# Optimization experiments

Measured on AMD Instinct MI355X. Metric: run time of the kernel, lower is better.

## Reference

```python
import jax, jax.numpy as jnp
import numpy as np

B, S, N_WIRES, EMBED_DIM, NUM_HEADS = 4, 2048, 8, 512, 8
D_K = EMBED_DIM // NUM_HEADS


def setup_inputs() -> dict:
    key = jax.random.key(0)
    k_x, k_th, k_q, k_k, k_v, k_c = jax.random.split(key, 6)
    x = jax.random.normal(k_x, (B, S, N_WIRES), dtype=jnp.float32)
    # trainable RX rotation angles, one per wire
    theta = jax.random.normal(k_th, (N_WIRES,), dtype=jnp.float32) * 0.1
    # nn.Linear(n_wires, embed_dim, bias=False) weights have shape (embed_dim, n_wires)
    sc_in = 1.0 / np.sqrt(N_WIRES)
    Wq = jax.random.normal(k_q, (EMBED_DIM, N_WIRES), dtype=jnp.float32) * sc_in
    Wk = jax.random.normal(k_k, (EMBED_DIM, N_WIRES), dtype=jnp.float32) * sc_in
    Wv = jax.random.normal(k_v, (EMBED_DIM, N_WIRES), dtype=jnp.float32) * sc_in
    Wc = jax.random.normal(k_c, (EMBED_DIM, EMBED_DIM), dtype=jnp.float32) * (1.0 / np.sqrt(EMBED_DIM))
    return {"x": x, "theta": theta, "Wq": Wq, "Wk": Wk, "Wv": Wv, "Wc": Wc}


def reference(x, theta, Wq, Wk, Wv, Wc):
    # Quantum encoding closed form: RX(x_i) then RX(theta_i) on |0> per wire gives <Z> = cos(x_i + theta_i).
    proj = jnp.cos(x + theta)  # (B, S, n_wires)
    b, s, _ = proj.shape
    q = jnp.einsum('bsn,en->bse', proj, Wq)
    k = jnp.einsum('bsn,en->bse', proj, Wk)
    v = jnp.einsum('bsn,en->bse', proj, Wv)
    # split heads: (B, H, S, d_k)
    q = q.reshape(b, s, NUM_HEADS, D_K).transpose(0, 2, 1, 3)
    k = k.reshape(b, s, NUM_HEADS, D_K).transpose(0, 2, 1, 3)
    v = v.reshape(b, s, NUM_HEADS, D_K).transpose(0, 2, 1, 3)
    scores = jnp.einsum('bhqd,bhkd->bhqk', q, k) / np.sqrt(D_K).astype(np.float32)
    attn = jax.nn.softmax(scores, axis=-1)  # dropout is identity at inference
    out = jnp.einsum('bhqk,bhkd->bhqd', attn, v)
    out = out.transpose(0, 2, 1, 3).reshape(b, s, EMBED_DIM)
    return jnp.einsum('bse,fe->bsf', out, Wc)
```

## Files before the change

### kernel.cpp

```cpp
#include <hip/hip_runtime.h>
#include <stdint.h>

#define N_B 4
#define S_LEN 2048
#define N_H 8
#define E_DIM 512

typedef __attribute__((ext_vector_type(8))) short bf16x8;
typedef __attribute__((ext_vector_type(4))) float f32x4;
typedef __attribute__((ext_vector_type(4))) unsigned int u32x4;
typedef __attribute__((ext_vector_type(2))) unsigned int u32x2;
typedef __attribute__((ext_vector_type(4))) unsigned short u16x4;
typedef __attribute__((ext_vector_type(8))) unsigned short u16x8;

#define MFMA16(a, b, c) __builtin_amdgcn_mfma_f32_16x16x32_bf16((a), (b), (c), 0, 0, 0)

__device__ __forceinline__ unsigned short f2bf(float f) {
    union { float f; unsigned int u; } v; v.f = f;
    unsigned int r = v.u + 0x7fffu + ((v.u >> 16) & 1u);
    return (unsigned short)(r >> 16);
}

__device__ __forceinline__ unsigned int pack2bf(float lo, float hi) {
    union { float f; unsigned int u; } a, b; a.f = lo; b.f = hi;
    return __builtin_amdgcn_perm(b.u + 0x8000u, a.u + 0x8000u, 0x07060302u);
}

__device__ __forceinline__ float fexp2(float x) {
#if __has_builtin(__builtin_amdgcn_exp2f)
    return __builtin_amdgcn_exp2f(x);
#else
    return exp2f(x);
#endif
}

#define Q_SCALE 0.18033688f

__global__ __launch_bounds__(256) void qkv_kernel(
    const float* __restrict__ x, const float* __restrict__ theta,
    const float* __restrict__ Wq, const float* __restrict__ Wk,
    const float* __restrict__ Wv,
    unsigned short* __restrict__ Q, unsigned short* __restrict__ K,
    unsigned short* __restrict__ Vt)
{
    __shared__ float proj[32][8];
    const int tid = threadIdx.x;
    const int mat = blockIdx.x % 3;
    const int chunk = blockIdx.x / 3;
    const int row0 = chunk * 32;
    const int b = row0 >> 11;
    const int s_in_b = row0 & (S_LEN - 1);

    proj[tid >> 3][tid & 7] = cosf(x[row0 * 8 + tid] + theta[tid & 7]);
    __syncthreads();

    if (mat < 2) {
        const float* W = (mat == 0) ? Wq : Wk;
        const float scale = (mat == 0) ? Q_SCALE : 1.0f;
        unsigned short* outp = (mat == 0) ? Q : K;
        const int eg = (tid & 127) * 4;
        const int sg = (tid >> 7) * 16;
        float w[4][8];
        #pragma unroll
        for (int e = 0; e < 4; ++e)
            #pragma unroll
            for (int n = 0; n < 8; ++n)
                w[e][n] = W[(eg + e) * 8 + n] * scale;
        const int h = eg >> 6, d0 = eg & 63;
        unsigned short* p0 = outp + ((size_t)(b * N_H + h) * S_LEN + s_in_b + sg) * 64 + d0;
        #pragma unroll 4
        for (int s = 0; s < 16; ++s) {
            f32x4 pa = *(const f32x4*)&proj[sg + s][0];
            f32x4 pc = *(const f32x4*)&proj[sg + s][4];
            u16x4 o;
            #pragma unroll
            for (int e = 0; e < 4; ++e) {
                float a = 0.f;
                #pragma unroll
                for (int n = 0; n < 4; ++n)
                    a += pa[n] * w[e][n] + pc[n] * w[e][n + 4];
                o[e] = f2bf(a);
            }
            *(u16x4*)&p0[s * 64] = o;
        }
    } else {
        f32x4 ps[8][2];
        const int sl0 = (tid & 3) * 8;
        #pragma unroll
        for (int k2 = 0; k2 < 8; ++k2) {
            ps[k2][0] = *(const f32x4*)&proj[sl0 + k2][0];
            ps[k2][1] = *(const f32x4*)&proj[sl0 + k2][4];
        }
        const int ecol = tid >> 2;
        for (int pass = 0; pass < 8; ++pass) {
            const int e = pass * 64 + ecol;
            const int h = e >> 6, dd = e & 63;
            float wr[8];
            #pragma unroll
            for (int n = 0; n < 8; ++n) wr[n] = Wv[e * 8 + n];
            u16x8 pk;
            #pragma unroll
            for (int k2 = 0; k2 < 8; ++k2) {
                float acc = 0.f;
                #pragma unroll
                for (int n = 0; n < 4; ++n)
                    acc += ps[k2][0][n] * wr[n] + ps[k2][1][n] * wr[n + 4];
                pk[k2] = f2bf(acc);
            }
            *(u16x8*)&Vt[((size_t)(b * N_H + h) * 64 + dd) * S_LEN + s_in_b + sl0] = pk;
        }
    }
}

__global__ __launch_bounds__(256, 4) void flash_kernel(
    const unsigned short* __restrict__ Q, const unsigned short* __restrict__ K,
    const unsigned short* __restrict__ Vt, unsigned short* __restrict__ O)
{
    __shared__ short kt[64 * 72];
    __shared__ short vt[64 * 72];
    __shared__ short pb[128 * 72];

    const int tid = threadIdx.x;
    const int lane = tid & 63, w = tid >> 6;
    const int quad = lane >> 4, lq = lane & 15;
    const int qt = blockIdx.x & 15, bh = blockIdx.x >> 4;
    const int b = bh >> 3, h = bh & 7;

    const unsigned short* Qb = Q + (size_t)bh * S_LEN * 64;
    const unsigned short* Kb = K + (size_t)bh * S_LEN * 64;
    const unsigned short* Vb = Vt + (size_t)bh * 64 * S_LEN;

    bf16x8 qf[2][2];
    #pragma unroll
    for (int mt = 0; mt < 2; ++mt)
        #pragma unroll
        for (int ks = 0; ks < 2; ++ks)
            qf[mt][ks] = *(const bf16x8*)&Qb[(size_t)(qt * 128 + w * 32 + mt * 16 + lq) * 64 + ks * 32 + quad * 8];

    f32x4 oacc[2][4];
    #pragma unroll
    for (int mt = 0; mt < 2; ++mt)
        #pragma unroll
        for (int dt = 0; dt < 4; ++dt) oacc[mt][dt] = 0.f;
    float lsum[2] = {0.f, 0.f};

    u32x4 pkr[2], pvr[2];
    #pragma unroll
    for (int i = 0; i < 2; ++i) {
        const int u = tid + (i << 8);
        pkr[i] = *(const u32x4*)&Kb[(size_t)(u >> 3) * 64 + (u & 7) * 8];
        pvr[i] = *(const u32x4*)&Vb[(size_t)(u >> 3) * S_LEN + (u & 7) * 8];
    }

    for (int kti = 0; kti < 32; ++kti) {
        __syncthreads();
        #pragma unroll
        for (int i = 0; i < 2; ++i) {
            const int u = tid + (i << 8);
            *(u32x4*)&kt[(u >> 3) * 72 + (u & 7) * 8] = pkr[i];
            *(u32x4*)&vt[(u >> 3) * 72 + (u & 7) * 8] = pvr[i];
        }
        __syncthreads();

        const int kb2 = (kti < 31) ? (kti + 1) * 64 : 0;
        #pragma unroll
        for (int i = 0; i < 2; ++i) {
            const int u = tid + (i << 8);
            pkr[i] = *(const u32x4*)&Kb[(size_t)(kb2 + (u >> 3)) * 64 + (u & 7) * 8];
            pvr[i] = *(const u32x4*)&Vb[(size_t)(u >> 3) * S_LEN + kb2 + (u & 7) * 8];
        }

        f32x4 sacc[2][4];
        #pragma unroll
        for (int mt = 0; mt < 2; ++mt)
            #pragma unroll
            for (int mts = 0; mts < 4; ++mts) sacc[mt][mts] = 0.f;
        #pragma unroll
        for (int mts = 0; mts < 4; ++mts) {
            #pragma unroll
            for (int ks = 0; ks < 2; ++ks) {
                bf16x8 af = *(const bf16x8*)&kt[(mts * 16 + lq) * 72 + ks * 32 + quad * 8];
                sacc[0][mts] = MFMA16(af, qf[0][ks], sacc[0][mts]);
                sacc[1][mts] = MFMA16(af, qf[1][ks], sacc[1][mts]);
            }
        }

        #pragma unroll
        for (int mt = 0; mt < 2; ++mt) {
            #pragma unroll
            for (int mts = 0; mts < 4; ++mts) {
                f32x4 p;
                #pragma unroll
                for (int e = 0; e < 4; ++e) p[e] = fexp2(sacc[mt][mts][e]);
                lsum[mt] += (p[0] + p[1]) + (p[2] + p[3]);
                u32x2 pw = { pack2bf(p[0], p[1]), pack2bf(p[2], p[3]) };
                *(u32x2*)&pb[(w * 32 + mt * 16 + lq) * 72 + mts * 16 + quad * 4] = pw;
            }
        }

        #pragma unroll
        for (int ks = 0; ks < 2; ++ks) {
            bf16x8 af0 = *(const bf16x8*)&pb[(w * 32 + lq) * 72 + ks * 32 + quad * 8];
            bf16x8 af1 = *(const bf16x8*)&pb[(w * 32 + 16 + lq) * 72 + ks * 32 + quad * 8];
            #pragma unroll
            for (int dt = 0; dt < 4; ++dt) {
                bf16x8 bf = *(const bf16x8*)&vt[(dt * 16 + lq) * 72 + ks * 32 + quad * 8];
                oacc[0][dt] = MFMA16(af0, bf, oacc[0][dt]);
                oacc[1][dt] = MFMA16(af1, bf, oacc[1][dt]);
            }
        }
    }

    #pragma unroll
    for (int mt = 0; mt < 2; ++mt) {
        float rs = lsum[mt];
        rs += __shfl_xor(rs, 16);
        rs += __shfl_xor(rs, 32);
        const float inv = 1.0f / rs;
        #pragma unroll
        for (int r = 0; r < 4; ++r) {
            const float ir = __shfl(inv, quad * 4 + r);
            const int row = qt * 128 + w * 32 + mt * 16 + quad * 4 + r;
            unsigned short* dst = &O[((size_t)b * S_LEN + row) * E_DIM + h * 64];
            #pragma unroll
            for (int dt = 0; dt < 4; ++dt)
                dst[dt * 16 + lq] = f2bf(oacc[mt][dt][r] * ir);
        }
    }
}

__global__ __launch_bounds__(256, 4) void outproj_kernel(
    const unsigned short* __restrict__ O, const float* __restrict__ Wc,
    float* __restrict__ Y)
{
    __shared__ short at[64 * 72];
    __shared__ short bt[64 * 72];
    const int tid = threadIdx.x;
    const int lane = tid & 63, w = tid >> 6;
    const int quad = lane >> 4, lq = lane & 15;
    const int m0 = (blockIdx.x >> 3) * 64;
    const int f0 = (blockIdx.x & 7) * 64;

    f32x4 acc[4];
    #pragma unroll
    for (int nt = 0; nt < 4; ++nt) acc[nt] = 0.f;

    u32x4 pa[2];
    f32x4 pw[4];
    #pragma unroll
    for (int i = 0; i < 2; ++i) {
        const int u = tid + (i << 8);
        pa[i] = *(const u32x4*)&O[(size_t)(m0 + (u >> 3)) * E_DIM + (u & 7) * 8];
    }
    #pragma unroll
    for (int i = 0; i < 4; ++i) {
        const int u = tid + (i << 8);
        pw[i] = *(const f32x4*)&Wc[(size_t)(f0 + (u >> 4)) * E_DIM + (u & 15) * 4];
    }

    for (int e0 = 0; e0 < E_DIM; e0 += 64) {
        __syncthreads();
        #pragma unroll
        for (int i = 0; i < 2; ++i) {
            const int u = tid + (i << 8);
            *(u32x4*)&at[(u >> 3) * 72 + (u & 7) * 8] = pa[i];
        }
        #pragma unroll
        for (int i = 0; i < 4; ++i) {
            const int u = tid + (i << 8);
            u16x4 pk = { f2bf(pw[i][0]), f2bf(pw[i][1]), f2bf(pw[i][2]), f2bf(pw[i][3]) };
            *(u16x4*)&bt[(u >> 4) * 72 + (u & 15) * 4] = pk;
        }
        __syncthreads();

        const int e1 = (e0 + 64 < E_DIM) ? e0 + 64 : 0;
        #pragma unroll
        for (int i = 0; i < 2; ++i) {
            const int u = tid + (i << 8);
            pa[i] = *(const u32x4*)&O[(size_t)(m0 + (u >> 3)) * E_DIM + e1 + (u & 7) * 8];
        }
        #pragma unroll
        for (int i = 0; i < 4; ++i) {
            const int u = tid + (i << 8);
            pw[i] = *(const f32x4*)&Wc[(size_t)(f0 + (u >> 4)) * E_DIM + e1 + (u & 15) * 4];
        }

        bf16x8 afk[2];
        #pragma unroll
        for (int ks = 0; ks < 2; ++ks)
            afk[ks] = *(const bf16x8*)&at[(w * 16 + lq) * 72 + ks * 32 + quad * 8];
        #pragma unroll
        for (int nt = 0; nt < 4; ++nt) {
            #pragma unroll
            for (int ks = 0; ks < 2; ++ks) {
                bf16x8 bf = *(const bf16x8*)&bt[(nt * 16 + lq) * 72 + ks * 32 + quad * 8];
                acc[nt] = MFMA16(afk[ks], bf, acc[nt]);
            }
        }
    }

    #pragma unroll
    for (int nt = 0; nt < 4; ++nt)
        #pragma unroll
        for (int r = 0; r < 4; ++r)
            Y[(size_t)(m0 + w * 16 + quad * 4 + r) * E_DIM + f0 + nt * 16 + lq] = acc[nt][r];
}

extern "C" void kernel_launch(void* const* d_in, const int* in_sizes, int n_in,
                              void* d_out, int out_size, void* d_ws, size_t ws_size,
                              hipStream_t stream) {
    const float* x     = (const float*)d_in[0];
    const float* theta = (const float*)d_in[1];
    const float* Wq    = (const float*)d_in[2];
    const float* Wk    = (const float*)d_in[3];
    const float* Wv    = (const float*)d_in[4];
    const float* Wc    = (const float*)d_in[5];
    float* Y = (float*)d_out;

    char* ws = (char*)d_ws;
    unsigned short* Q  = (unsigned short*)(ws);
    unsigned short* K  = (unsigned short*)(ws + ((size_t)8 << 20));
    unsigned short* Vt = (unsigned short*)(ws + ((size_t)16 << 20));
    unsigned short* O  = (unsigned short*)(ws + ((size_t)24 << 20));

    qkv_kernel<<<(N_B * S_LEN / 32) * 3, 256, 0, stream>>>(x, theta, Wq, Wk, Wv, Q, K, Vt);
    flash_kernel<<<N_B * N_H * (S_LEN / 128), 256, 0, stream>>>(Q, K, Vt, O);
    outproj_kernel<<<(N_B * S_LEN / 64) * (E_DIM / 64), 256, 0, stream>>>(O, Wc, Y);
}
```

Baseline: 142.0 us.

## Keep P in registers via transposed PV MFMA and restructure output projection

The flash kernel now computes the transposed output O^T = V^T P^T with 16x16x16 MFMAs, so the exponentiated score fragments feed the MFMA straight from registers. This removes the shared-memory P buffer and its write/read round trip. LDS padding drops to 66 shorts, launch bounds are relaxed to 2 blocks per CU, and the output store becomes vectorized 4-wide bf16. The output projection kernel now loads a full 64x512 bf16 slice of Wc into LDS once per block, reads O fragments directly from global memory, and covers 256 rows per block; this gives fewer blocks and less repeated Wc conversion, at the cost of uncoalesced-looking global A loads and a large LDS footprint.

New measurement: 160.0 us. 12.7% more time.

```diff
diff --git a/kernel.cpp b/kernel.cpp
--- a/kernel.cpp
+++ b/kernel.cpp
@@ -7,6 +7,7 @@
 #define E_DIM 512
 
 typedef __attribute__((ext_vector_type(8))) short bf16x8;
+typedef __attribute__((ext_vector_type(4))) short bf16x4;
 typedef __attribute__((ext_vector_type(4))) float f32x4;
 typedef __attribute__((ext_vector_type(4))) unsigned int u32x4;
 typedef __attribute__((ext_vector_type(2))) unsigned int u32x2;
@@ -14,6 +15,7 @@
 typedef __attribute__((ext_vector_type(8))) unsigned short u16x8;
 
 #define MFMA16(a, b, c) __builtin_amdgcn_mfma_f32_16x16x32_bf16((a), (b), (c), 0, 0, 0)
+#define MFMA16K16(a, b, c) __builtin_amdgcn_mfma_f32_16x16x16bf16_1k((a), (b), (c), 0, 0, 0)
 
 __device__ __forceinline__ unsigned short f2bf(float f) {
     union { float f; unsigned int u; } v; v.f = f;
@@ -24,14 +26,6 @@
 __device__ __forceinline__ unsigned int pack2bf(float lo, float hi) {
     union { float f; unsigned int u; } a, b; a.f = lo; b.f = hi;
     return __builtin_amdgcn_perm(b.u + 0x8000u, a.u + 0x8000u, 0x07060302u);
-}
-
-__device__ __forceinline__ float fexp2(float x) {
-#if __has_builtin(__builtin_amdgcn_exp2f)
-    return __builtin_amdgcn_exp2f(x);
-#else
-    return exp2f(x);
-#endif
 }
 
 #define Q_SCALE 0.18033688f
@@ -112,13 +106,12 @@
     }
 }
 
-__global__ __launch_bounds__(256, 4) void flash_kernel(
+__global__ __launch_bounds__(256, 2) void flash_kernel(
     const unsigned short* __restrict__ Q, const unsigned short* __restrict__ K,
     const unsigned short* __restrict__ Vt, unsigned short* __restrict__ O)
 {
-    __shared__ short kt[64 * 72];
-    __shared__ short vt[64 * 72];
-    __shared__ short pb[128 * 72];
+    __shared__ short kt[64 * 66];
+    __shared__ short vt[64 * 66];
 
     const int tid = threadIdx.x;
     const int lane = tid & 63, w = tid >> 6;
@@ -137,11 +130,11 @@
         for (int ks = 0; ks < 2; ++ks)
             qf[mt][ks] = *(const bf16x8*)&Qb[(size_t)(qt * 128 + w * 32 + mt * 16 + lq) * 64 + ks * 32 + quad * 8];
 
-    f32x4 oacc[2][4];
+    f32x4 oT[2][4];
     #pragma unroll
     for (int mt = 0; mt < 2; ++mt)
         #pragma unroll
-        for (int dt = 0; dt < 4; ++dt) oacc[mt][dt] = 0.f;
+        for (int dblk = 0; dblk < 4; ++dblk) oT[mt][dblk] = 0.f;
     float lsum[2] = {0.f, 0.f};
 
     u32x4 pkr[2], pvr[2];
@@ -157,8 +150,8 @@
         #pragma unroll
         for (int i = 0; i < 2; ++i) {
             const int u = tid + (i << 8);
-            *(u32x4*)&kt[(u >> 3) * 72 + (u & 7) * 8] = pkr[i];
-            *(u32x4*)&vt[(u >> 3) * 72 + (u & 7) * 8] = pvr[i];
+            *(u32x4*)&kt[(u >> 3) * 66 + (u & 7) * 8] = pkr[i];
+            *(u32x4*)&vt[(u >> 3) * 66 + (u & 7) * 8] = pvr[i];
         }
         __syncthreads();
 
@@ -179,34 +172,35 @@
         for (int mts = 0; mts < 4; ++mts) {
             #pragma unroll
             for (int ks = 0; ks < 2; ++ks) {
-                bf16x8 af = *(const bf16x8*)&kt[(mts * 16 + lq) * 72 + ks * 32 + quad * 8];
+                bf16x8 af = *(const bf16x8*)&kt[(mts * 16 + lq) * 66 + ks * 32 + quad * 8];
                 sacc[0][mts] = MFMA16(af, qf[0][ks], sacc[0][mts]);
                 sacc[1][mts] = MFMA16(af, qf[1][ks], sacc[1][mts]);
             }
         }
 
+        bf16x4 pfrag[2][4];
         #pragma unroll
         for (int mt = 0; mt < 2; ++mt) {
             #pragma unroll
             for (int mts = 0; mts < 4; ++mts) {
                 f32x4 p;
                 #pragma unroll
-                for (int e = 0; e < 4; ++e) p[e] = fexp2(sacc[mt][mts][e]);
+                for (int e = 0; e < 4; ++e) p[e] = exp2f(sacc[mt][mts][e]);
                 lsum[mt] += (p[0] + p[1]) + (p[2] + p[3]);
-                u32x2 pw = { pack2bf(p[0], p[1]), pack2bf(p[2], p[3]) };
-                *(u32x2*)&pb[(w * 32 + mt * 16 + lq) * 72 + mts * 16 + quad * 4] = pw;
-            }
-        }
-
-        #pragma unroll
-        for (int ks = 0; ks < 2; ++ks) {
-            bf16x8 af0 = *(const bf16x8*)&pb[(w * 32 + lq) * 72 + ks * 32 + quad * 8];
-            bf16x8 af1 = *(const bf16x8*)&pb[(w * 32 + 16 + lq) * 72 + ks * 32 + quad * 8];
-            #pragma unroll
-            for (int dt = 0; dt < 4; ++dt) {
-                bf16x8 bf = *(const bf16x8*)&vt[(dt * 16 + lq) * 72 + ks * 32 + quad * 8];
-                oacc[0][dt] = MFMA16(af0, bf, oacc[0][dt]);
-                oacc[1][dt] = MFMA16(af1, bf, oacc[1][dt]);
+                union { u32x2 u; bf16x4 s; } cv;
+                cv.u[0] = pack2bf(p[0], p[1]);
+                cv.u[1] = pack2bf(p[2], p[3]);
+                pfrag[mt][mts] = cv.s;
+            }
+        }
+
+        #pragma unroll
+        for (int dblk = 0; dblk < 4; ++dblk) {
+            #pragma unroll
+            for (int mts = 0; mts < 4; ++mts) {
+                bf16x4 vf = *(const bf16x4*)&vt[(dblk * 16 + lq) * 66 + mts * 16 + quad * 4];
+                oT[0][dblk] = MFMA16K16(vf, pfrag[0][mts], oT[0][dblk]);
+                oT[1][dblk] = MFMA16K16(vf, pfrag[1][mts], oT[1][dblk]);
             }
         }
     }
@@ -217,93 +211,70 @@
         rs += __shfl_xor(rs, 16);
         rs += __shfl_xor(rs, 32);
         const float inv = 1.0f / rs;
-        #pragma unroll
-        for (int r = 0; r < 4; ++r) {
-            const float ir = __shfl(inv, quad * 4 + r);
-            const int row = qt * 128 + w * 32 + mt * 16 + quad * 4 + r;
-            unsigned short* dst = &O[((size_t)b * S_LEN + row) * E_DIM + h * 64];
-            #pragma unroll
-            for (int dt = 0; dt < 4; ++dt)
-                dst[dt * 16 + lq] = f2bf(oacc[mt][dt][r] * ir);
-        }
-    }
-}
-
-__global__ __launch_bounds__(256, 4) void outproj_kernel(
+        const int q = qt * 128 + w * 32 + mt * 16 + lq;
+        unsigned short* dst = &O[((size_t)b * S_LEN + q) * E_DIM + h * 64];
+        #pragma unroll
+        for (int dblk = 0; dblk < 4; ++dblk) {
+            u16x4 o;
+            #pragma unroll
+            for (int r = 0; r < 4; ++r) o[r] = f2bf(oT[mt][dblk][r] * inv);
+            *(u16x4*)&dst[dblk * 16 + quad * 4] = o;
+        }
+    }
+}
+
+__global__ __launch_bounds__(256) void outproj_kernel(
     const unsigned short* __restrict__ O, const float* __restrict__ Wc,
     float* __restrict__ Y)
 {
-    __shared__ short at[64 * 72];
-    __shared__ short bt[64 * 72];
+    __shared__ short wl[64 * 514];
     const int tid = threadIdx.x;
     const int lane = tid & 63, w = tid >> 6;
     const int quad = lane >> 4, lq = lane & 15;
-    const int m0 = (blockIdx.x >> 3) * 64;
     const int f0 = (blockIdx.x & 7) * 64;
-
-    f32x4 acc[4];
-    #pragma unroll
-    for (int nt = 0; nt < 4; ++nt) acc[nt] = 0.f;
-
-    u32x4 pa[2];
-    f32x4 pw[4];
-    #pragma unroll
-    for (int i = 0; i < 2; ++i) {
+    const int m0 = (blockIdx.x >> 3) * 256;
+
+    #pragma unroll
+    for (int i = 0; i < 32; ++i) {
         const int u = tid + (i << 8);
-        pa[i] = *(const u32x4*)&O[(size_t)(m0 + (u >> 3)) * E_DIM + (u & 7) * 8];
-    }
-    #pragma unroll
-    for (int i = 0; i < 4; ++i) {
-        const int u = tid + (i << 8);
-        pw[i] = *(const f32x4*)&Wc[(size_t)(f0 + (u >> 4)) * E_DIM + (u & 15) * 4];
-    }
-
-    for (int e0 = 0; e0 < E_DIM; e0 += 64) {
-        __syncthreads();
-        #pragma unroll
-        for (int i = 0; i < 2; ++i) {
-            const int u = tid + (i << 8);
-            *(u32x4*)&at[(u >> 3) * 72 + (u & 7) * 8] = pa[i];
-        }
-        #pragma unroll
-        for (int i = 0; i < 4; ++i) {
-            const int u = tid + (i << 8);
-            u16x4 pk = { f2bf(pw[i][0]), f2bf(pw[i][1]), f2bf(pw[i][2]), f2bf(pw[i][3]) };
-            *(u16x4*)&bt[(u >> 4) * 72 + (u & 15) * 4] = pk;
-        }
-        __syncthreads();
-
-        const int e1 = (e0 + 64 < E_DIM) ? e0 + 64 : 0;
-        #pragma unroll
-        for (int i = 0; i < 2; ++i) {
-            const int u = tid + (i << 8);
-            pa[i] = *(const u32x4*)&O[(size_t)(m0 + (u >> 3)) * E_DIM + e1 + (u & 7) * 8];
-        }
-        #pragma unroll
-        for (int i = 0; i < 4; ++i) {
-            const int u = tid + (i << 8);
-            pw[i] = *(const f32x4*)&Wc[(size_t)(f0 + (u >> 4)) * E_DIM + e1 + (u & 15) * 4];
-        }
-
-        bf16x8 afk[2];
-        #pragma unroll
-        for (int ks = 0; ks < 2; ++ks)
-            afk[ks] = *(const bf16x8*)&at[(w * 16 + lq) * 72 + ks * 32 + quad * 8];
-        #pragma unroll
-        for (int nt = 0; nt < 4; ++nt) {
-            #pragma unroll
-            for (int ks = 0; ks < 2; ++ks) {
-                bf16x8 bf = *(const bf16x8*)&bt[(nt * 16 + lq) * 72 + ks * 32 + quad * 8];
-                acc[nt] = MFMA16(afk[ks], bf, acc[nt]);
-            }
-        }
-    }
-
-    #pragma unroll
-    for (int nt = 0; nt < 4; ++nt)
-        #pragma unroll
-        for (int r = 0; r < 4; ++r)
-            Y[(size_t)(m0 + w * 16 + quad * 4 + r) * E_DIM + f0 + nt * 16 + lq] = acc[nt][r];
+        const int r = u >> 7, c4 = (u & 127) * 4;
+        f32x4 fv = *(const f32x4*)&Wc[(size_t)(f0 + r) * E_DIM + c4];
+        u16x4 pk = { f2bf(fv[0]), f2bf(fv[1]), f2bf(fv[2]), f2bf(fv[3]) };
+        *(u16x4*)&wl[r * 514 + c4] = pk;
+    }
+    __syncthreads();
+
+    #pragma unroll
+    for (int mo = 0; mo < 2; ++mo) {
+        const int mbase = m0 + w * 64 + mo * 32;
+        f32x4 acc[2][4];
+        #pragma unroll
+        for (int mt = 0; mt < 2; ++mt)
+            #pragma unroll
+            for (int nt = 0; nt < 4; ++nt) acc[mt][nt] = 0.f;
+
+        #pragma unroll 4
+        for (int ks = 0; ks < 16; ++ks) {
+            bf16x8 af[2];
+            #pragma unroll
+            for (int mt = 0; mt < 2; ++mt)
+                af[mt] = *(const bf16x8*)&O[(size_t)(mbase + mt * 16 + lq) * E_DIM + ks * 32 + quad * 8];
+            #pragma unroll
+            for (int nt = 0; nt < 4; ++nt) {
+                bf16x8 bf = *(const bf16x8*)&wl[(nt * 16 + lq) * 514 + ks * 32 + quad * 8];
+                acc[0][nt] = MFMA16(af[0], bf, acc[0][nt]);
+                acc[1][nt] = MFMA16(af[1], bf, acc[1][nt]);
+            }
+        }
+
+        #pragma unroll
+        for (int mt = 0; mt < 2; ++mt)
+            #pragma unroll
+            for (int nt = 0; nt < 4; ++nt)
+                #pragma unroll
+                for (int r = 0; r < 4; ++r)
+                    Y[(size_t)(mbase + mt * 16 + quad * 4 + r) * E_DIM + f0 + nt * 16 + lq] = acc[mt][nt][r];
+    }
 }
 
 extern "C" void kernel_launch(void* const* d_in, const int* in_sizes, int n_in,
@@ -325,5 +296,5 @@
 
     qkv_kernel<<<(N_B * S_LEN / 32) * 3, 256, 0, stream>>>(x, theta, Wq, Wk, Wv, Q, K, Vt);
     flash_kernel<<<N_B * N_H * (S_LEN / 128), 256, 0, stream>>>(Q, K, Vt, O);
-    outproj_kernel<<<(N_B * S_LEN / 64) * (E_DIM / 64), 256, 0, stream>>>(O, Wc, Y);
-}
+    outproj_kernel<<<(N_B * S_LEN / 256) * (E_DIM / 64), 256, 0, stream>>>(O, Wc, Y);
+}
```
